# Optimization experiments

Measured on AMD Instinct MI355X. Metric: run time of the kernel, lower is better.

## Reference

```python
import jax, jax.numpy as jnp
import numpy as np

NUM_HEADS = 8
LOCAL_WINDOW = 32


def setup_inputs() -> dict:
    key = jax.random.key(0)
    ks = jax.random.split(key, 5)
    B, T, D = 2, 2048, 512
    s = 1.0 / np.sqrt(D)
    return {
        "x": jax.random.normal(ks[0], (B, T, D), dtype=jnp.float32),
        "Wq": jax.random.normal(ks[1], (D, D), dtype=jnp.float32) * s,
        "bq": jnp.zeros((D,), dtype=jnp.float32),
        "Wk": jax.random.normal(ks[2], (D, D), dtype=jnp.float32) * s,
        "bk": jnp.zeros((D,), dtype=jnp.float32),
        "Wv": jax.random.normal(ks[3], (D, D), dtype=jnp.float32) * s,
        "bv": jnp.zeros((D,), dtype=jnp.float32),
        "Wo": jax.random.normal(ks[4], (D, D), dtype=jnp.float32) * s,
        "bo": jnp.zeros((D,), dtype=jnp.float32),
    }


def reference(x, Wq, bq, Wk, bk, Wv, bv, Wo, bo):
    B, T, D = x.shape
    H = NUM_HEADS
    hd = D // H
    scale = hd ** -0.5
    w = LOCAL_WINDOW

    def proj(W, b):
        # (B,T,D) -> (B,H,T,hd)
        return (x @ W.T + b).reshape(B, T, H, hd).transpose(0, 2, 1, 3)

    q = proj(Wq, bq)
    k = proj(Wk, bk)
    v = proj(Wv, bv)

    scores = jnp.einsum("bhqd,bhkd->bhqk", q, k) * scale  # (B,H,T,T)

    if w < T:
        i = jnp.arange(T)[:, None]
        j = jnp.arange(T)[None, :]
        # row i attends to columns [i - w//2, i + w//2)  (end exclusive)
        allowed = (j >= i - w // 2) & (j < i + w // 2)  # (T,T)
        scores = jnp.where(allowed[None, None], scores, jnp.float32(-jnp.inf))

    attn = jax.nn.softmax(scores, axis=-1)
    out = jnp.einsum("bhqk,bhkd->bhqd", attn, v)  # (B,H,T,hd)
    out = out.transpose(0, 2, 1, 3).reshape(B, T, D)
    return out @ Wo.T + bo
```

## Files before the change

kernel.cpp:

```cpp
#include <hip/hip_runtime.h>

#define B_  2
#define T_  2048
#define D_  512
#define H_  8
#define HD_ 64
#define WHALF_ 16
#define Mtot (B_*T_)
#define QKV_LD 1536

typedef __attribute__((ext_vector_type(8))) short short8;
typedef __attribute__((ext_vector_type(4))) short short4v;
typedef __attribute__((ext_vector_type(4))) float floatx4;

__device__ __forceinline__ unsigned short f2bf(float f) {
    unsigned u = __float_as_uint(f);
    u = (u + 0x7fffu + ((u >> 16) & 1u)) >> 16;
    return (unsigned short)u;
}

__device__ __forceinline__ void glds16(const unsigned short* g, unsigned short* l) {
    __builtin_amdgcn_global_load_lds(
        (const __attribute__((address_space(1))) void*)g,
        (__attribute__((address_space(3))) void*)l, 16, 0, 0);
}

__global__ __launch_bounds__(256) void cast_all(
    const float* __restrict__ x,
    const float* __restrict__ Wq, const float* __restrict__ Wk,
    const float* __restrict__ Wv, const float* __restrict__ Wo,
    const float* __restrict__ bq, const float* __restrict__ bk,
    const float* __restrict__ bv,
    unsigned short* __restrict__ xb,
    unsigned short* __restrict__ wqkv, unsigned short* __restrict__ wob,
    float* __restrict__ bqkv)
{
    if (blockIdx.x < 2048) {
        int i = blockIdx.x * 256 + threadIdx.x;
        float4 f = ((const float4*)x)[i];
        ushort4 o;
        o.x = f2bf(f.x); o.y = f2bf(f.y); o.z = f2bf(f.z); o.w = f2bf(f.w);
        ((ushort4*)xb)[i] = o;
    } else if (blockIdx.x < 3072) {
        int gid = (blockIdx.x - 2048) * 256 + threadIdx.x;
        int m   = gid >> 16;
        int idx = gid & 0xFFFF;
        const float* src = (m == 0) ? Wq : (m == 1) ? Wk : (m == 2) ? Wv : Wo;
        float4 f = ((const float4*)src)[idx];
        ushort4 o;
        o.x = f2bf(f.x); o.y = f2bf(f.y); o.z = f2bf(f.z); o.w = f2bf(f.w);
        if (m < 3) ((ushort4*)wqkv)[(m << 16) + idx] = o;
        else       ((ushort4*)wob)[idx] = o;
    } else {
        for (int i = threadIdx.x; i < 384; i += 256) {
            const float* src = (i < 128) ? bq : (i < 256) ? bk : bv;
            ((float4*)bqkv)[i] = ((const float4*)src)[i & 127];
        }
    }
}

__global__ __launch_bounds__(256) void gemm_qkv(
    const unsigned short* __restrict__ A, const unsigned short* __restrict__ W,
    const float* __restrict__ bias, unsigned short* __restrict__ C)
{
    __shared__ unsigned short As[64 * 64];
    __shared__ unsigned short Bs[64 * 64];

    const int t  = threadIdx.x;
    const int m0 = blockIdx.x * 64;
    const int n0 = blockIdx.y * 64;
    const int w  = t >> 6, l = t & 63;
    const int quad = l >> 4, lo = l & 15;

    const int lr = l >> 3;
    const int csw = ((l & 7) ^ lr) * 8;
    const unsigned short* Ag[2]; unsigned short* ldsA[2];
    const unsigned short* Bg[2]; unsigned short* ldsB[2];
    #pragma unroll
    for (int p = 0; p < 2; ++p) {
        Ag[p] = A + (size_t)(m0 + 16 * w + 8 * p + lr) * 512 + csw;
        ldsA[p] = &As[(16 * w + 8 * p) * 64];
        Bg[p] = W + (size_t)(n0 + 16 * w + 8 * p + lr) * 512 + csw;
        ldsB[p] = &Bs[(16 * w + 8 * p) * 64];
    }

    floatx4 acc[4];
    #pragma unroll
    for (int j = 0; j < 4; ++j) acc[j] = (floatx4)0.0f;

    const int swlo = lo & 7;

    for (int k0 = 0; k0 < 512; k0 += 64) {
        #pragma unroll
        for (int p = 0; p < 2; ++p) { glds16(Ag[p] + k0, ldsA[p]); glds16(Bg[p] + k0, ldsB[p]); }
        __syncthreads();

        #pragma unroll
        for (int ks = 0; ks < 2; ++ks) {
            const int cg = ((ks * 4 + quad) ^ swlo) * 8;
            short8 a = *(const short8*)(&As[(w * 16 + lo) * 64 + cg]);
            #pragma unroll
            for (int j = 0; j < 4; ++j) {
                short8 b = *(const short8*)(&Bs[(j * 16 + lo) * 64 + cg]);
                acc[j] = __builtin_amdgcn_mfma_f32_16x16x32_bf16(a, b, acc[j], 0, 0, 0);
            }
        }
        __syncthreads();
    }

    #pragma unroll
    for (int j = 0; j < 4; ++j) {
        int col = n0 + j * 16 + lo;
        float bv = bias[col];
        #pragma unroll
        for (int r = 0; r < 4; ++r) {
            int row = m0 + w * 16 + quad * 4 + r;
            C[(size_t)row * QKV_LD + col] = f2bf(acc[j][r] + bv);
        }
    }
}

__global__ __launch_bounds__(256) void gemm_out(
    const unsigned short* __restrict__ attb, const unsigned short* __restrict__ wob,
    const float* __restrict__ bo, float* __restrict__ out)
{
    __shared__ unsigned short As[64 * 64];
    __shared__ unsigned short Bs[64 * 64];

    const int t  = threadIdx.x;
    const int m0 = blockIdx.x * 64;
    const int n0 = blockIdx.y * 64;
    const int w  = t >> 6, l = t & 63;
    const int quad = l >> 4, lo = l & 15;

    const int lr = l >> 3;
    const int csw = ((l & 7) ^ lr) * 8;
    const unsigned short* Ag[2]; unsigned short* ldsA[2];
    const unsigned short* Bg[2]; unsigned short* ldsB[2];
    #pragma unroll
    for (int p = 0; p < 2; ++p) {
        Ag[p] = attb + (size_t)(m0 + 16 * w + 8 * p + lr) * 512 + csw;
        ldsA[p] = &As[(16 * w + 8 * p) * 64];
        Bg[p] = wob + (size_t)(n0 + 16 * w + 8 * p + lr) * 512 + csw;
        ldsB[p] = &Bs[(16 * w + 8 * p) * 64];
    }

    floatx4 acc[4];
    #pragma unroll
    for (int j = 0; j < 4; ++j) acc[j] = (floatx4)0.0f;

    const int swlo = lo & 7;

    for (int k0 = 0; k0 < 512; k0 += 64) {
        #pragma unroll
        for (int p = 0; p < 2; ++p) { glds16(Ag[p] + k0, ldsA[p]); glds16(Bg[p] + k0, ldsB[p]); }
        __syncthreads();

        #pragma unroll
        for (int ks = 0; ks < 2; ++ks) {
            const int cg = ((ks * 4 + quad) ^ swlo) * 8;
            short8 a = *(const short8*)(&As[(w * 16 + lo) * 64 + cg]);
            #pragma unroll
            for (int j = 0; j < 4; ++j) {
                short8 b = *(const short8*)(&Bs[(j * 16 + lo) * 64 + cg]);
                acc[j] = __builtin_amdgcn_mfma_f32_16x16x32_bf16(a, b, acc[j], 0, 0, 0);
            }
        }
        __syncthreads();
    }

    #pragma unroll
    for (int j = 0; j < 4; ++j) {
        int col = n0 + j * 16 + lo;
        float bv = bo[col];
        #pragma unroll
        for (int r = 0; r < 4; ++r) {
            int row = m0 + w * 16 + quad * 4 + r;
            out[(size_t)row * 512 + col] = acc[j][r] + bv;
        }
    }
}

#define QLD 72
#define VLD 76

__global__ __launch_bounds__(256) void attn_mfma(
    const unsigned short* __restrict__ qkv, unsigned short* __restrict__ att)
{
    __shared__ unsigned short Qs[64][QLD];
    __shared__ unsigned short Ks[96][QLD];
    __shared__ unsigned short Vs[96][VLD];
    __shared__ unsigned short Pws[4][16][QLD];

    const int q0 = blockIdx.x * 64;
    const int bh = blockIdx.y;
    const int b = bh >> 3, h = bh & 7;
    const int t = threadIdx.x;
    const int wq = t >> 6, l = t & 63;
    const int quad = l >> 4, lo = l & 15;

    const size_t baseQ = (size_t)(b * T_) * QKV_LD + h * HD_;

    for (int c = t; c < 512; c += 256) {
        int row = c >> 3, cg = c & 7;
        *(short8*)(&Qs[row][cg * 8]) =
            *(const short8*)(&qkv[baseQ + (size_t)(q0 + row) * QKV_LD + cg * 8]);
    }
    for (int c = t; c < 768; c += 256) {
        int row = c >> 3, cg = c & 7;
        int g = q0 - WHALF_ + row;
        short8 kv = (short8)(short)0;
        if (g >= 0 && g < T_)
            kv = *(const short8*)(&qkv[baseQ + 512 + (size_t)g * QKV_LD + cg * 8]);
        *(short8*)(&Ks[row][cg * 8]) = kv;
    }
    for (int c = t; c < 768; c += 256) {
        int row = c >> 3, cg = c & 7;
        int g = q0 - WHALF_ + row;
        short8 vv = (short8)(short)0;
        if (g >= 0 && g < T_)
            vv = *(const short8*)(&qkv[baseQ + 1024 + (size_t)g * QKV_LD + cg * 8]);
        short4v lo4 = { vv[0], vv[1], vv[2], vv[3] };
        short4v hi4 = { vv[4], vv[5], vv[6], vv[7] };
        *(short4v*)(&Vs[row][cg * 8])     = lo4;
        *(short4v*)(&Vs[row][cg * 8 + 4]) = hi4;
    }
    __syncthreads();

    const int ks0 = wq >> 1;
    const int kb  = ks0 * 2;

    floatx4 S[4];
    #pragma unroll
    for (int tt = 0; tt < 4; ++tt) S[tt] = (floatx4)0.0f;
    short8 aq[2];
    #pragma unroll
    for (int ks = 0; ks < 2; ++ks)
        aq[ks] = *(const short8*)(&Qs[wq * 16 + lo][ks * 32 + quad * 8]);
    #pragma unroll
    for (int tt = 0; tt < 4; ++tt) {
        #pragma unroll
        for (int ks = 0; ks < 2; ++ks) {
            short8 bk8 = *(const short8*)(&Ks[(kb + tt) * 16 + lo][ks * 32 + quad * 8]);
            S[tt] = __builtin_amdgcn_mfma_f32_16x16x32_bf16(aq[ks], bk8, S[tt], 0, 0, 0);
        }
    }

    float inv_r[4];
    #pragma unroll
    for (int r = 0; r < 4; ++r) {
        int qi = q0 + wq * 16 + quad * 4 + r;
        float mx = -1e30f;
        float sv[4]; bool vd[4];
        #pragma unroll
        for (int tt = 0; tt < 4; ++tt) {
            int j = q0 - WHALF_ + (kb + tt) * 16 + lo;
            bool ok = (j >= qi - WHALF_) && (j < qi + WHALF_) && (j >= 0) && (j < T_);
            float s = S[tt][r] * 0.125f;
            sv[tt] = s; vd[tt] = ok;
            mx = (ok && s > mx) ? s : mx;
        }
        #pragma unroll
        for (int mm = 1; mm < 16; mm <<= 1) mx = fmaxf(mx, __shfl_xor(mx, mm, 16));
        float den = 0.f;
        #pragma unroll
        for (int tt = 0; tt < 4; ++tt) {
            float e = vd[tt] ? __expf(sv[tt] - mx) : 0.f;
            Pws[wq][quad * 4 + r][tt * 16 + lo] = f2bf(e);
            den += e;
        }
        #pragma unroll
        for (int mm = 1; mm < 16; mm <<= 1) den += __shfl_xor(den, mm, 16);
        inv_r[r] = 1.0f / den;
    }

    floatx4 O[4];
    #pragma unroll
    for (int nt = 0; nt < 4; ++nt) O[nt] = (floatx4)0.0f;
    #pragma unroll
    for (int ksr = 0; ksr < 2; ++ksr) {
        short8 ap = *(const short8*)(&Pws[wq][lo][ksr * 32 + quad * 8]);
        const int krow = (ks0 + ksr) * 32 + quad * 8;
        #pragma unroll
        for (int nt = 0; nt < 4; ++nt) {
            short8 bv8;
            #pragma unroll
            for (int j = 0; j < 8; ++j)
                bv8[j] = (short)Vs[krow + j][nt * 16 + lo];
            O[nt] = __builtin_amdgcn_mfma_f32_16x16x32_bf16(ap, bv8, O[nt], 0, 0, 0);
        }
    }

    #pragma unroll
    for (int r = 0; r < 4; ++r) {
        int qi = q0 + wq * 16 + quad * 4 + r;
        size_t rowb = (size_t)(b * T_ + qi) * D_ + h * HD_;
        #pragma unroll
        for (int nt = 0; nt < 4; ++nt)
            att[rowb + nt * 16 + lo] = f2bf(O[nt][r] * inv_r[r]);
    }
}

extern "C" void kernel_launch(void* const* d_in, const int* in_sizes, int n_in,
                              void* d_out, int out_size, void* d_ws, size_t ws_size,
                              hipStream_t stream) {
    const float* x  = (const float*)d_in[0];
    const float* Wq = (const float*)d_in[1];
    const float* bq = (const float*)d_in[2];
    const float* Wk = (const float*)d_in[3];
    const float* bk = (const float*)d_in[4];
    const float* Wv = (const float*)d_in[5];
    const float* bv = (const float*)d_in[6];
    const float* Wo = (const float*)d_in[7];
    const float* bo = (const float*)d_in[8];
    float* out = (float*)d_out;

    char* ws = (char*)d_ws;
    unsigned short* xb   = (unsigned short*)(ws);
    unsigned short* wqkv = (unsigned short*)(ws +  4194304);
    unsigned short* wob  = (unsigned short*)(ws +  5767168);
    float*          bqkv = (float*)         (ws +  6291456);
    unsigned short* qkvb = (unsigned short*)(ws +  6297600);
    unsigned short* attb = (unsigned short*)(ws + 18880512);

    cast_all<<<3073, 256, 0, stream>>>(x, Wq, Wk, Wv, Wo, bq, bk, bv,
                                       xb, wqkv, wob, bqkv);

    gemm_qkv<<<dim3(Mtot / 64, QKV_LD / 64), 256, 0, stream>>>(
        xb, wqkv, bqkv, qkvb);

    attn_mfma<<<dim3(T_ / 64, B_ * H_), 256, 0, stream>>>(qkvb, attb);

    gemm_out<<<dim3(Mtot / 64, D_ / 64), 256, 0, stream>>>(attb, wob, bo, out);
}
```

Baseline: 106.4 us.

## Use 128x128 tiles with 2x2 warp layout for projection GEMMs

Merges the QKV and output projection GEMMs into one templated kernel that computes 128x128 output tiles, each wave owning a 64x64 sub-tile with 4x4 MFMA accumulators. This raises operand reuse from LDS and cuts global loads per flop. In exchange, grid sizes shrink by four, so the output projection launches only 128 blocks, and register pressure rises from the 16 accumulators.

Result: slower. 109.1 us (+2.5%).

```diff
diff --git a/kernel.cpp b/kernel.cpp
--- a/kernel.cpp
+++ b/kernel.cpp
@@ -59,124 +59,78 @@
     }
 }
 
-__global__ __launch_bounds__(256) void gemm_qkv(
+template<int CLD, int OUTF32>
+__global__ __launch_bounds__(256) void gemm128(
     const unsigned short* __restrict__ A, const unsigned short* __restrict__ W,
-    const float* __restrict__ bias, unsigned short* __restrict__ C)
+    const float* __restrict__ bias,
+    unsigned short* __restrict__ Cb, float* __restrict__ Cf)
 {
-    __shared__ unsigned short As[64 * 64];
-    __shared__ unsigned short Bs[64 * 64];
+    __shared__ unsigned short As[128 * 64];
+    __shared__ unsigned short Bs[128 * 64];
 
     const int t  = threadIdx.x;
-    const int m0 = blockIdx.x * 64;
-    const int n0 = blockIdx.y * 64;
+    const int m0 = blockIdx.x * 128;
+    const int n0 = blockIdx.y * 128;
     const int w  = t >> 6, l = t & 63;
     const int quad = l >> 4, lo = l & 15;
 
-    const int lr = l >> 3;
+    const int lr  = l >> 3;
     const int csw = ((l & 7) ^ lr) * 8;
-    const unsigned short* Ag[2]; unsigned short* ldsA[2];
-    const unsigned short* Bg[2]; unsigned short* ldsB[2];
-    #pragma unroll
-    for (int p = 0; p < 2; ++p) {
-        Ag[p] = A + (size_t)(m0 + 16 * w + 8 * p + lr) * 512 + csw;
-        ldsA[p] = &As[(16 * w + 8 * p) * 64];
-        Bg[p] = W + (size_t)(n0 + 16 * w + 8 * p + lr) * 512 + csw;
-        ldsB[p] = &Bs[(16 * w + 8 * p) * 64];
-    }
-
-    floatx4 acc[4];
-    #pragma unroll
-    for (int j = 0; j < 4; ++j) acc[j] = (floatx4)0.0f;
-
+    const unsigned short* Ag[4]; unsigned short* ldsA[4];
+    const unsigned short* Bg[4]; unsigned short* ldsB[4];
+    #pragma unroll
+    for (int p = 0; p < 4; ++p) {
+        Ag[p]   = A + (size_t)(m0 + 32 * w + 8 * p + lr) * 512 + csw;
+        ldsA[p] = &As[(32 * w + 8 * p) * 64];
+        Bg[p]   = W + (size_t)(n0 + 32 * w + 8 * p + lr) * 512 + csw;
+        ldsB[p] = &Bs[(32 * w + 8 * p) * 64];
+    }
+
+    floatx4 acc[4][4];
+    #pragma unroll
+    for (int m = 0; m < 4; ++m)
+        #pragma unroll
+        for (int n = 0; n < 4; ++n) acc[m][n] = (floatx4)0.0f;
+
+    const int wr = w >> 1, wc = w & 1;
     const int swlo = lo & 7;
 
     for (int k0 = 0; k0 < 512; k0 += 64) {
         #pragma unroll
-        for (int p = 0; p < 2; ++p) { glds16(Ag[p] + k0, ldsA[p]); glds16(Bg[p] + k0, ldsB[p]); }
+        for (int p = 0; p < 4; ++p) { glds16(Ag[p] + k0, ldsA[p]); glds16(Bg[p] + k0, ldsB[p]); }
         __syncthreads();
 
         #pragma unroll
         for (int ks = 0; ks < 2; ++ks) {
             const int cg = ((ks * 4 + quad) ^ swlo) * 8;
-            short8 a = *(const short8*)(&As[(w * 16 + lo) * 64 + cg]);
-            #pragma unroll
-            for (int j = 0; j < 4; ++j) {
-                short8 b = *(const short8*)(&Bs[(j * 16 + lo) * 64 + cg]);
-                acc[j] = __builtin_amdgcn_mfma_f32_16x16x32_bf16(a, b, acc[j], 0, 0, 0);
+            short8 a[4], b[4];
+            #pragma unroll
+            for (int m = 0; m < 4; ++m)
+                a[m] = *(const short8*)(&As[(wr * 64 + m * 16 + lo) * 64 + cg]);
+            #pragma unroll
+            for (int n = 0; n < 4; ++n)
+                b[n] = *(const short8*)(&Bs[(wc * 64 + n * 16 + lo) * 64 + cg]);
+            #pragma unroll
+            for (int m = 0; m < 4; ++m)
+                #pragma unroll
+                for (int n = 0; n < 4; ++n)
+                    acc[m][n] = __builtin_amdgcn_mfma_f32_16x16x32_bf16(a[m], b[n], acc[m][n], 0, 0, 0);
+        }
+        __syncthreads();
+    }
+
+    #pragma unroll
+    for (int n = 0; n < 4; ++n) {
+        int col = n0 + wc * 64 + n * 16 + lo;
+        float bv = bias[col];
+        #pragma unroll
+        for (int m = 0; m < 4; ++m) {
+            #pragma unroll
+            for (int r = 0; r < 4; ++r) {
+                int row = m0 + wr * 64 + m * 16 + quad * 4 + r;
+                if (OUTF32) Cf[(size_t)row * CLD + col] = acc[m][n][r] + bv;
+                else        Cb[(size_t)row * CLD + col] = f2bf(acc[m][n][r] + bv);
             }
-        }
-        __syncthreads();
-    }
-
-    #pragma unroll
-    for (int j = 0; j < 4; ++j) {
-        int col = n0 + j * 16 + lo;
-        float bv = bias[col];
-        #pragma unroll
-        for (int r = 0; r < 4; ++r) {
-            int row = m0 + w * 16 + quad * 4 + r;
-            C[(size_t)row * QKV_LD + col] = f2bf(acc[j][r] + bv);
-        }
-    }
-}
-
-__global__ __launch_bounds__(256) void gemm_out(
-    const unsigned short* __restrict__ attb, const unsigned short* __restrict__ wob,
-    const float* __restrict__ bo, float* __restrict__ out)
-{
-    __shared__ unsigned short As[64 * 64];
-    __shared__ unsigned short Bs[64 * 64];
-
-    const int t  = threadIdx.x;
-    const int m0 = blockIdx.x * 64;
-    const int n0 = blockIdx.y * 64;
-    const int w  = t >> 6, l = t & 63;
-    const int quad = l >> 4, lo = l & 15;
-
-    const int lr = l >> 3;
-    const int csw = ((l & 7) ^ lr) * 8;
-    const unsigned short* Ag[2]; unsigned short* ldsA[2];
-    const unsigned short* Bg[2]; unsigned short* ldsB[2];
-    #pragma unroll
-    for (int p = 0; p < 2; ++p) {
-        Ag[p] = attb + (size_t)(m0 + 16 * w + 8 * p + lr) * 512 + csw;
-        ldsA[p] = &As[(16 * w + 8 * p) * 64];
-        Bg[p] = wob + (size_t)(n0 + 16 * w + 8 * p + lr) * 512 + csw;
-        ldsB[p] = &Bs[(16 * w + 8 * p) * 64];
-    }
-
-    floatx4 acc[4];
-    #pragma unroll
-    for (int j = 0; j < 4; ++j) acc[j] = (floatx4)0.0f;
-
-    const int swlo = lo & 7;
-
-    for (int k0 = 0; k0 < 512; k0 += 64) {
-        #pragma unroll
-        for (int p = 0; p < 2; ++p) { glds16(Ag[p] + k0, ldsA[p]); glds16(Bg[p] + k0, ldsB[p]); }
-        __syncthreads();
-
-        #pragma unroll
-        for (int ks = 0; ks < 2; ++ks) {
-            const int cg = ((ks * 4 + quad) ^ swlo) * 8;
-            short8 a = *(const short8*)(&As[(w * 16 + lo) * 64 + cg]);
-            #pragma unroll
-            for (int j = 0; j < 4; ++j) {
-                short8 b = *(const short8*)(&Bs[(j * 16 + lo) * 64 + cg]);
-                acc[j] = __builtin_amdgcn_mfma_f32_16x16x32_bf16(a, b, acc[j], 0, 0, 0);
-            }
-        }
-        __syncthreads();
-    }
-
-    #pragma unroll
-    for (int j = 0; j < 4; ++j) {
-        int col = n0 + j * 16 + lo;
-        float bv = bo[col];
-        #pragma unroll
-        for (int r = 0; r < 4; ++r) {
-            int row = m0 + w * 16 + quad * 4 + r;
-            out[(size_t)row * 512 + col] = acc[j][r] + bv;
         }
     }
 }
@@ -326,10 +280,11 @@
     cast_all<<<3073, 256, 0, stream>>>(x, Wq, Wk, Wv, Wo, bq, bk, bv,
                                        xb, wqkv, wob, bqkv);
 
-    gemm_qkv<<<dim3(Mtot / 64, QKV_LD / 64), 256, 0, stream>>>(
-        xb, wqkv, bqkv, qkvb);
+    gemm128<QKV_LD, 0><<<dim3(Mtot / 128, QKV_LD / 128), 256, 0, stream>>>(
+        xb, wqkv, bqkv, qkvb, nullptr);
 
     attn_mfma<<<dim3(T_ / 64, B_ * H_), 256, 0, stream>>>(qkvb, attb);
 
-    gemm_out<<<dim3(Mtot / 64, D_ / 64), 256, 0, stream>>>(attb, wob, bo, out);
-}
+    gemm128<D_, 1><<<dim3(Mtot / 128, D_ / 128), 256, 0, stream>>>(
+        attb, wob, bo, nullptr, out);
+}
```

## Fuse QKV projection into local-attention kernel and retile output GEMM

Applied to the files above, without the earlier changes.

Removes the separate QKV GEMM and its bf16 intermediate buffer. Each attention block now computes its own Q (64 rows) and K/V (96 rows, including halo) for one head directly from x and the weights in LDS, then runs the windowed softmax attention in place. This avoids a global write and read of the QKV tensor and one kernel launch. The cost is recomputing K/V for the 32 halo rows of every block (about 1.5x K/V projection work) and uneven per-wave MFMA load. The output GEMM is also retiled so each wave computes a 2x2 block of 16x16 tiles.

New measurement: 101.5 us. 4.6% less time.

```diff
diff --git a/kernel.cpp b/kernel.cpp
--- a/kernel.cpp
+++ b/kernel.cpp
@@ -7,7 +7,6 @@
 #define HD_ 64
 #define WHALF_ 16
 #define Mtot (B_*T_)
-#define QKV_LD 1536
 
 typedef __attribute__((ext_vector_type(8))) short short8;
 typedef __attribute__((ext_vector_type(4))) short short4v;
@@ -33,7 +32,7 @@
     const float* __restrict__ bv,
     unsigned short* __restrict__ xb,
     unsigned short* __restrict__ wqkv, unsigned short* __restrict__ wob,
-    float* __restrict__ bqkv)
+    float* __restrict__ bqkv, unsigned short* __restrict__ zb)
 {
     if (blockIdx.x < 2048) {
         int i = blockIdx.x * 256 + threadIdx.x;
@@ -56,67 +55,229 @@
             const float* src = (i < 128) ? bq : (i < 256) ? bk : bv;
             ((float4*)bqkv)[i] = ((const float4*)src)[i & 127];
         }
-    }
-}
-
-__global__ __launch_bounds__(256) void gemm_qkv(
-    const unsigned short* __restrict__ A, const unsigned short* __restrict__ W,
-    const float* __restrict__ bias, unsigned short* __restrict__ C)
+        if (threadIdx.x < 128) {
+            float4 z; z.x = 0.f; z.y = 0.f; z.z = 0.f; z.w = 0.f;
+            ((float4*)zb)[threadIdx.x] = z;
+        }
+    }
+}
+
+#define QLD 72
+#define VLD 76
+
+__global__ __launch_bounds__(256) void qkv_attn(
+    const unsigned short* __restrict__ xb,
+    const unsigned short* __restrict__ wqkv,
+    const float* __restrict__ bqkv,
+    const unsigned short* __restrict__ zb,
+    unsigned short* __restrict__ att)
 {
-    __shared__ unsigned short As[64 * 64];
-    __shared__ unsigned short Bs[64 * 64];
-
-    const int t  = threadIdx.x;
-    const int m0 = blockIdx.x * 64;
-    const int n0 = blockIdx.y * 64;
-    const int w  = t >> 6, l = t & 63;
+    __shared__ unsigned short S[288 * 64];
+    __shared__ unsigned short Qs[64][QLD];
+    __shared__ unsigned short Ks[96][QLD];
+    __shared__ unsigned short Vs[96][VLD];
+
+    const int q0 = blockIdx.x * 64;
+    const int bh = blockIdx.y;
+    const int b = bh >> 3, h = bh & 7;
+    const int t = threadIdx.x;
+    const int w = t >> 6, l = t & 63;
     const int quad = l >> 4, lo = l & 15;
-
-    const int lr = l >> 3;
+    const int lr  = l >> 3;
     const int csw = ((l & 7) ^ lr) * 8;
-    const unsigned short* Ag[2]; unsigned short* ldsA[2];
-    const unsigned short* Bg[2]; unsigned short* ldsB[2];
-    #pragma unroll
-    for (int p = 0; p < 2; ++p) {
-        Ag[p] = A + (size_t)(m0 + 16 * w + 8 * p + lr) * 512 + csw;
-        ldsA[p] = &As[(16 * w + 8 * p) * 64];
-        Bg[p] = W + (size_t)(n0 + 16 * w + 8 * p + lr) * 512 + csw;
-        ldsB[p] = &Bs[(16 * w + 8 * p) * 64];
-    }
-
-    floatx4 acc[4];
-    #pragma unroll
-    for (int j = 0; j < 4; ++j) acc[j] = (floatx4)0.0f;
-
-    const int swlo = lo & 7;
+
+    const unsigned short* src[9];
+    unsigned short* dst[9];
+    #pragma unroll
+    for (int i = 0; i < 9; ++i) {
+        int c = w * 9 + i;
+        dst[i] = &S[c * 512];
+        if (c < 12) {
+            int g0 = q0 - 16 + 8 * c;
+            src[i] = (g0 >= 0 && g0 < T_)
+                   ? (xb + (size_t)(b * T_ + g0 + lr) * 512 + csw)
+                   : (zb + csw);
+        } else {
+            int wr0 = (c - 12) * 8;
+            int m = wr0 >> 6;
+            int r = (wr0 & 63) + lr;
+            src[i] = wqkv + (size_t)m * 262144 + (size_t)(h * 64 + r) * 512 + csw;
+        }
+    }
+
+    floatx4 acc[4][4];
+    #pragma unroll
+    for (int m = 0; m < 4; ++m)
+        #pragma unroll
+        for (int n = 0; n < 4; ++n) acc[m][n] = (floatx4)0.0f;
+
+    const int swlo = lo & 15 & 7;
 
     for (int k0 = 0; k0 < 512; k0 += 64) {
         #pragma unroll
-        for (int p = 0; p < 2; ++p) { glds16(Ag[p] + k0, ldsA[p]); glds16(Bg[p] + k0, ldsB[p]); }
+        for (int i = 0; i < 9; ++i) glds16(src[i] + k0, dst[i]);
         __syncthreads();
 
         #pragma unroll
         for (int ks = 0; ks < 2; ++ks) {
             const int cg = ((ks * 4 + quad) ^ swlo) * 8;
-            short8 a = *(const short8*)(&As[(w * 16 + lo) * 64 + cg]);
-            #pragma unroll
-            for (int j = 0; j < 4; ++j) {
-                short8 b = *(const short8*)(&Bs[(j * 16 + lo) * 64 + cg]);
-                acc[j] = __builtin_amdgcn_mfma_f32_16x16x32_bf16(a, b, acc[j], 0, 0, 0);
+            if (w != 3) {
+                const int ab = (w == 0) ? 16 : 0;
+                const int bb = 96 + (w << 6);
+                short8 a[4], bf[4];
+                #pragma unroll
+                for (int m = 0; m < 4; ++m)
+                    a[m] = *(const short8*)(&S[(ab + m * 16 + lo) * 64 + cg]);
+                #pragma unroll
+                for (int n = 0; n < 4; ++n)
+                    bf[n] = *(const short8*)(&S[(bb + n * 16 + lo) * 64 + cg]);
+                #pragma unroll
+                for (int m = 0; m < 4; ++m)
+                    #pragma unroll
+                    for (int n = 0; n < 4; ++n)
+                        acc[m][n] = __builtin_amdgcn_mfma_f32_16x16x32_bf16(a[m], bf[n], acc[m][n], 0, 0, 0);
+            } else {
+                short8 a2[2], bk4[4], bv4[4];
+                #pragma unroll
+                for (int j = 0; j < 2; ++j)
+                    a2[j] = *(const short8*)(&S[(64 + j * 16 + lo) * 64 + cg]);
+                #pragma unroll
+                for (int n = 0; n < 4; ++n) {
+                    bk4[n] = *(const short8*)(&S[(160 + n * 16 + lo) * 64 + cg]);
+                    bv4[n] = *(const short8*)(&S[(224 + n * 16 + lo) * 64 + cg]);
+                }
+                #pragma unroll
+                for (int n = 0; n < 4; ++n) {
+                    acc[0][n] = __builtin_amdgcn_mfma_f32_16x16x32_bf16(a2[0], bk4[n], acc[0][n], 0, 0, 0);
+                    acc[1][n] = __builtin_amdgcn_mfma_f32_16x16x32_bf16(a2[1], bk4[n], acc[1][n], 0, 0, 0);
+                    acc[2][n] = __builtin_amdgcn_mfma_f32_16x16x32_bf16(a2[0], bv4[n], acc[2][n], 0, 0, 0);
+                    acc[3][n] = __builtin_amdgcn_mfma_f32_16x16x32_bf16(a2[1], bv4[n], acc[3][n], 0, 0, 0);
+                }
             }
         }
         __syncthreads();
     }
 
-    #pragma unroll
-    for (int j = 0; j < 4; ++j) {
-        int col = n0 + j * 16 + lo;
-        float bv = bias[col];
-        #pragma unroll
-        for (int r = 0; r < 4; ++r) {
-            int row = m0 + w * 16 + quad * 4 + r;
-            C[(size_t)row * QKV_LD + col] = f2bf(acc[j][r] + bv);
-        }
+    if (w == 0) {
+        #pragma unroll
+        for (int n = 0; n < 4; ++n) {
+            float bb = bqkv[h * 64 + n * 16 + lo];
+            #pragma unroll
+            for (int m = 0; m < 4; ++m)
+                #pragma unroll
+                for (int r = 0; r < 4; ++r)
+                    Qs[m * 16 + quad * 4 + r][n * 16 + lo] = f2bf(acc[m][n][r] + bb);
+        }
+    } else if (w == 1) {
+        #pragma unroll
+        for (int n = 0; n < 4; ++n) {
+            float bb = bqkv[512 + h * 64 + n * 16 + lo];
+            #pragma unroll
+            for (int m = 0; m < 4; ++m)
+                #pragma unroll
+                for (int r = 0; r < 4; ++r)
+                    Ks[m * 16 + quad * 4 + r][n * 16 + lo] = f2bf(acc[m][n][r] + bb);
+        }
+    } else if (w == 2) {
+        #pragma unroll
+        for (int n = 0; n < 4; ++n) {
+            float bb = bqkv[1024 + h * 64 + n * 16 + lo];
+            #pragma unroll
+            for (int m = 0; m < 4; ++m)
+                #pragma unroll
+                for (int r = 0; r < 4; ++r)
+                    Vs[m * 16 + quad * 4 + r][n * 16 + lo] = f2bf(acc[m][n][r] + bb);
+        }
+    } else {
+        #pragma unroll
+        for (int n = 0; n < 4; ++n) {
+            float bbk = bqkv[512  + h * 64 + n * 16 + lo];
+            float bbv = bqkv[1024 + h * 64 + n * 16 + lo];
+            #pragma unroll
+            for (int j = 0; j < 2; ++j)
+                #pragma unroll
+                for (int r = 0; r < 4; ++r) {
+                    Ks[64 + j * 16 + quad * 4 + r][n * 16 + lo] = f2bf(acc[j][n][r] + bbk);
+                    Vs[64 + j * 16 + quad * 4 + r][n * 16 + lo] = f2bf(acc[2 + j][n][r] + bbv);
+                }
+        }
+    }
+    __syncthreads();
+
+    unsigned short (*Pws)[16][QLD] = (unsigned short (*)[16][QLD])S;
+
+    const int wq  = w;
+    const int ks0 = wq >> 1;
+    const int kb  = ks0 * 2;
+
+    floatx4 Sf[4];
+    #pragma unroll
+    for (int tt = 0; tt < 4; ++tt) Sf[tt] = (floatx4)0.0f;
+    short8 aq[2];
+    #pragma unroll
+    for (int ks = 0; ks < 2; ++ks)
+        aq[ks] = *(const short8*)(&Qs[wq * 16 + lo][ks * 32 + quad * 8]);
+    #pragma unroll
+    for (int tt = 0; tt < 4; ++tt) {
+        #pragma unroll
+        for (int ks = 0; ks < 2; ++ks) {
+            short8 bk8 = *(const short8*)(&Ks[(kb + tt) * 16 + lo][ks * 32 + quad * 8]);
+            Sf[tt] = __builtin_amdgcn_mfma_f32_16x16x32_bf16(aq[ks], bk8, Sf[tt], 0, 0, 0);
+        }
+    }
+
+    float inv_r[4];
+    #pragma unroll
+    for (int r = 0; r < 4; ++r) {
+        int qi = q0 + wq * 16 + quad * 4 + r;
+        float mx = -1e30f;
+        float sv[4]; bool vd[4];
+        #pragma unroll
+        for (int tt = 0; tt < 4; ++tt) {
+            int j = q0 - WHALF_ + (kb + tt) * 16 + lo;
+            bool ok = (j >= qi - WHALF_) && (j < qi + WHALF_) && (j >= 0) && (j < T_);
+            float s = Sf[tt][r] * 0.125f;
+            sv[tt] = s; vd[tt] = ok;
+            mx = (ok && s > mx) ? s : mx;
+        }
+        #pragma unroll
+        for (int mm = 1; mm < 16; mm <<= 1) mx = fmaxf(mx, __shfl_xor(mx, mm, 16));
+        float den = 0.f;
+        #pragma unroll
+        for (int tt = 0; tt < 4; ++tt) {
+            float e = vd[tt] ? __expf(sv[tt] - mx) : 0.f;
+            Pws[wq][quad * 4 + r][tt * 16 + lo] = f2bf(e);
+            den += e;
+        }
+        #pragma unroll
+        for (int mm = 1; mm < 16; mm <<= 1) den += __shfl_xor(den, mm, 16);
+        inv_r[r] = 1.0f / den;
+    }
+
+    floatx4 O[4];
+    #pragma unroll
+    for (int nt = 0; nt < 4; ++nt) O[nt] = (floatx4)0.0f;
+    #pragma unroll
+    for (int ksr = 0; ksr < 2; ++ksr) {
+        short8 ap = *(const short8*)(&Pws[wq][lo][ksr * 32 + quad * 8]);
+        const int krow = (ks0 + ksr) * 32 + quad * 8;
+        #pragma unroll
+        for (int nt = 0; nt < 4; ++nt) {
+            short8 bv8;
+            #pragma unroll
+            for (int j = 0; j < 8; ++j)
+                bv8[j] = (short)Vs[krow + j][nt * 16 + lo];
+            O[nt] = __builtin_amdgcn_mfma_f32_16x16x32_bf16(ap, bv8, O[nt], 0, 0, 0);
+        }
+    }
+
+    #pragma unroll
+    for (int r = 0; r < 4; ++r) {
+        int qi = q0 + wq * 16 + quad * 4 + r;
+        size_t rowb = (size_t)(b * T_ + qi) * D_ + h * HD_;
+        #pragma unroll
+        for (int nt = 0; nt < 4; ++nt)
+            att[rowb + nt * 16 + lo] = f2bf(O[nt][r] * inv_r[r]);
     }
 }
 
@@ -145,10 +306,13 @@
         ldsB[p] = &Bs[(16 * w + 8 * p) * 64];
     }
 
-    floatx4 acc[4];
-    #pragma unroll
-    for (int j = 0; j < 4; ++j) acc[j] = (floatx4)0.0f;
-
+    floatx4 acc[2][2];
+    #pragma unroll
+    for (int m = 0; m < 2; ++m)
+        #pragma unroll
+        for (int n = 0; n < 2; ++n) acc[m][n] = (floatx4)0.0f;
+
+    const int wr = w >> 1, wc = w & 1;
     const int swlo = lo & 7;
 
     for (int k0 = 0; k0 < 512; k0 += 64) {
@@ -159,145 +323,34 @@
         #pragma unroll
         for (int ks = 0; ks < 2; ++ks) {
             const int cg = ((ks * 4 + quad) ^ swlo) * 8;
-            short8 a = *(const short8*)(&As[(w * 16 + lo) * 64 + cg]);
-            #pragma unroll
-            for (int j = 0; j < 4; ++j) {
-                short8 b = *(const short8*)(&Bs[(j * 16 + lo) * 64 + cg]);
-                acc[j] = __builtin_amdgcn_mfma_f32_16x16x32_bf16(a, b, acc[j], 0, 0, 0);
+            short8 a[2], bf[2];
+            #pragma unroll
+            for (int m = 0; m < 2; ++m)
+                a[m] = *(const short8*)(&As[(wr * 32 + m * 16 + lo) * 64 + cg]);
+            #pragma unroll
+            for (int n = 0; n < 2; ++n)
+                bf[n] = *(const short8*)(&Bs[(wc * 32 + n * 16 + lo) * 64 + cg]);
+            #pragma unroll
+            for (int m = 0; m < 2; ++m)
+                #pragma unroll
+                for (int n = 0; n < 2; ++n)
+                    acc[m][n] = __builtin_amdgcn_mfma_f32_16x16x32_bf16(a[m], bf[n], acc[m][n], 0, 0, 0);
+        }
+        __syncthreads();
+    }
+
+    #pragma unroll
+    for (int n = 0; n < 2; ++n) {
+        int col = n0 + wc * 32 + n * 16 + lo;
+        float bv = bo[col];
+        #pragma unroll
+        for (int m = 0; m < 2; ++m) {
+            #pragma unroll
+            for (int r = 0; r < 4; ++r) {
+                int row = m0 + wr * 32 + m * 16 + quad * 4 + r;
+                out[(size_t)row * 512 + col] = acc[m][n][r] + bv;
             }
         }
-        __syncthreads();
-    }
-
-    #pragma unroll
-    for (int j = 0; j < 4; ++j) {
-        int col = n0 + j * 16 + lo;
-        float bv = bo[col];
-        #pragma unroll
-        for (int r = 0; r < 4; ++r) {
-            int row = m0 + w * 16 + quad * 4 + r;
-            out[(size_t)row * 512 + col] = acc[j][r] + bv;
-        }
-    }
-}
-
-#define QLD 72
-#define VLD 76
-
-__global__ __launch_bounds__(256) void attn_mfma(
-    const unsigned short* __restrict__ qkv, unsigned short* __restrict__ att)
-{
-    __shared__ unsigned short Qs[64][QLD];
-    __shared__ unsigned short Ks[96][QLD];
-    __shared__ unsigned short Vs[96][VLD];
-    __shared__ unsigned short Pws[4][16][QLD];
-
-    const int q0 = blockIdx.x * 64;
-    const int bh = blockIdx.y;
-    const int b = bh >> 3, h = bh & 7;
-    const int t = threadIdx.x;
-    const int wq = t >> 6, l = t & 63;
-    const int quad = l >> 4, lo = l & 15;
-
-    const size_t baseQ = (size_t)(b * T_) * QKV_LD + h * HD_;
-
-    for (int c = t; c < 512; c += 256) {
-        int row = c >> 3, cg = c & 7;
-        *(short8*)(&Qs[row][cg * 8]) =
-            *(const short8*)(&qkv[baseQ + (size_t)(q0 + row) * QKV_LD + cg * 8]);
-    }
-    for (int c = t; c < 768; c += 256) {
-        int row = c >> 3, cg = c & 7;
-        int g = q0 - WHALF_ + row;
-        short8 kv = (short8)(short)0;
-        if (g >= 0 && g < T_)
-            kv = *(const short8*)(&qkv[baseQ + 512 + (size_t)g * QKV_LD + cg * 8]);
-        *(short8*)(&Ks[row][cg * 8]) = kv;
-    }
-    for (int c = t; c < 768; c += 256) {
-        int row = c >> 3, cg = c & 7;
-        int g = q0 - WHALF_ + row;
-        short8 vv = (short8)(short)0;
-        if (g >= 0 && g < T_)
-            vv = *(const short8*)(&qkv[baseQ + 1024 + (size_t)g * QKV_LD + cg * 8]);
-        short4v lo4 = { vv[0], vv[1], vv[2], vv[3] };
-        short4v hi4 = { vv[4], vv[5], vv[6], vv[7] };
-        *(short4v*)(&Vs[row][cg * 8])     = lo4;
-        *(short4v*)(&Vs[row][cg * 8 + 4]) = hi4;
-    }
-    __syncthreads();
-
-    const int ks0 = wq >> 1;
-    const int kb  = ks0 * 2;
-
-    floatx4 S[4];
-    #pragma unroll
-    for (int tt = 0; tt < 4; ++tt) S[tt] = (floatx4)0.0f;
-    short8 aq[2];
-    #pragma unroll
-    for (int ks = 0; ks < 2; ++ks)
-        aq[ks] = *(const short8*)(&Qs[wq * 16 + lo][ks * 32 + quad * 8]);
-    #pragma unroll
-    for (int tt = 0; tt < 4; ++tt) {
-        #pragma unroll
-        for (int ks = 0; ks < 2; ++ks) {
-            short8 bk8 = *(const short8*)(&Ks[(kb + tt) * 16 + lo][ks * 32 + quad * 8]);
-            S[tt] = __builtin_amdgcn_mfma_f32_16x16x32_bf16(aq[ks], bk8, S[tt], 0, 0, 0);
-        }
-    }
-
-    float inv_r[4];
-    #pragma unroll
-    for (int r = 0; r < 4; ++r) {
-        int qi = q0 + wq * 16 + quad * 4 + r;
-        float mx = -1e30f;
-        float sv[4]; bool vd[4];
-        #pragma unroll
-        for (int tt = 0; tt < 4; ++tt) {
-            int j = q0 - WHALF_ + (kb + tt) * 16 + lo;
-            bool ok = (j >= qi - WHALF_) && (j < qi + WHALF_) && (j >= 0) && (j < T_);
-            float s = S[tt][r] * 0.125f;
-            sv[tt] = s; vd[tt] = ok;
-            mx = (ok && s > mx) ? s : mx;
-        }
-        #pragma unroll
-        for (int mm = 1; mm < 16; mm <<= 1) mx = fmaxf(mx, __shfl_xor(mx, mm, 16));
-        float den = 0.f;
-        #pragma unroll
-        for (int tt = 0; tt < 4; ++tt) {
-            float e = vd[tt] ? __expf(sv[tt] - mx) : 0.f;
-            Pws[wq][quad * 4 + r][tt * 16 + lo] = f2bf(e);
-            den += e;
-        }
-        #pragma unroll
-        for (int mm = 1; mm < 16; mm <<= 1) den += __shfl_xor(den, mm, 16);
-        inv_r[r] = 1.0f / den;
-    }
-
-    floatx4 O[4];
-    #pragma unroll
-    for (int nt = 0; nt < 4; ++nt) O[nt] = (floatx4)0.0f;
-    #pragma unroll
-    for (int ksr = 0; ksr < 2; ++ksr) {
-        short8 ap = *(const short8*)(&Pws[wq][lo][ksr * 32 + quad * 8]);
-        const int krow = (ks0 + ksr) * 32 + quad * 8;
-        #pragma unroll
-        for (int nt = 0; nt < 4; ++nt) {
-            short8 bv8;
-            #pragma unroll
-            for (int j = 0; j < 8; ++j)
-                bv8[j] = (short)Vs[krow + j][nt * 16 + lo];
-            O[nt] = __builtin_amdgcn_mfma_f32_16x16x32_bf16(ap, bv8, O[nt], 0, 0, 0);
-        }
-    }
-
-    #pragma unroll
-    for (int r = 0; r < 4; ++r) {
-        int qi = q0 + wq * 16 + quad * 4 + r;
-        size_t rowb = (size_t)(b * T_ + qi) * D_ + h * HD_;
-        #pragma unroll
-        for (int nt = 0; nt < 4; ++nt)
-            att[rowb + nt * 16 + lo] = f2bf(O[nt][r] * inv_r[r]);
     }
 }
 
@@ -320,16 +373,14 @@
     unsigned short* wqkv = (unsigned short*)(ws +  4194304);
     unsigned short* wob  = (unsigned short*)(ws +  5767168);
     float*          bqkv = (float*)         (ws +  6291456);
-    unsigned short* qkvb = (unsigned short*)(ws +  6297600);
-    unsigned short* attb = (unsigned short*)(ws + 18880512);
+    unsigned short* zb   = (unsigned short*)(ws +  6297600);
+    unsigned short* attb = (unsigned short*)(ws +  6299648);
 
     cast_all<<<3073, 256, 0, stream>>>(x, Wq, Wk, Wv, Wo, bq, bk, bv,
-                                       xb, wqkv, wob, bqkv);
-
-    gemm_qkv<<<dim3(Mtot / 64, QKV_LD / 64), 256, 0, stream>>>(
-        xb, wqkv, bqkv, qkvb);
-
-    attn_mfma<<<dim3(T_ / 64, B_ * H_), 256, 0, stream>>>(qkvb, attb);
+                                       xb, wqkv, wob, bqkv, zb);
+
+    qkv_attn<<<dim3(T_ / 64, B_ * H_), 256, 0, stream>>>(
+        xb, wqkv, bqkv, zb, attb);
 
     gemm_out<<<dim3(Mtot / 64, D_ / 64), 256, 0, stream>>>(attb, wob, bo, out);
 }
```
